# Kernel tuning notes

Hardware: AMD Instinct MI355X
Metric: run time of the kernel (lower is better)

Reference implementation:

```python
import jax, jax.numpy as jnp
import numpy as np

WINDOW = 128  # causal window width
D_SCALE = None  # set from val dim at trace time


def _softsign(x):
    return x / (1.0 + jnp.abs(x))


def setup_inputs() -> dict:
    key = jax.random.key(0)
    k1, k2 = jax.random.split(key)
    B, N, D = 4, 4096, 256
    val = jax.random.normal(k1, (B, N, D), dtype=jnp.float32)
    state = jax.random.normal(k2, (B, N), dtype=jnp.float32)
    return {"val": val, "state": state}


def reference(val, state):
    # val: [B, N, D], state: [B, N]
    B, N, D = val.shape
    # pairwise_fn: scaled dot product -> scores [B, N, N]
    scores = jnp.einsum('bnd,bmd->bnm', val, val) / jnp.sqrt(jnp.asarray(D, val.dtype))
    # edge_compress_fn: softsign
    edges = _softsign(scores)
    # causal window mask: source j satisfies (j <= i) & (j >= i - window)
    i = jnp.arange(N)[:, None]
    j = jnp.arange(N)[None, :]
    mask = (j <= i) & (j >= i - WINDOW)  # [N, N]
    edges = edges * mask[None, :, :].astype(edges.dtype)
    # val_proj_fn / state_proj_fn are Identity
    delta_state = jnp.einsum('bij,bj->bi', edges, state)   # [B, N]
    delta_val = jnp.einsum('bij,bjd->bid', edges, val)      # [B, N, D]
    return (delta_state, delta_val)
```

## Files before the change

### kernel.cpp

```cpp
#include <hip/hip_runtime.h>

#define NSEQ 4096
#define DIM  256
#define WIN  128
#define BATCH 4

typedef __bf16 bf16x8 __attribute__((ext_vector_type(8)));
typedef float  f32x4  __attribute__((ext_vector_type(4)));
typedef int    v2i    __attribute__((ext_vector_type(2)));
typedef int    v4i    __attribute__((ext_vector_type(4)));

__device__ __forceinline__ int sub_off(int j, int d) {
    return (((j >> 2) * 16 + (d >> 4)) << 6) + ((j & 3) << 4) + (d & 15);
}

__device__ __forceinline__ unsigned short f2bf(float f) {
    unsigned u = __builtin_bit_cast(unsigned, f);
    u += 0x7fffu + ((u >> 16) & 1u);
    return (unsigned short)(u >> 16);
}

__device__ __forceinline__ unsigned pk2bf(float lo, float hi) {
    unsigned r;
    asm("v_cvt_pk_bf16_f32 %0, %1, %2" : "=v"(r) : "v"(lo), "v"(hi));
    return r;
}

__global__ __launch_bounds__(256, 3)
void sp_kernel(const float* __restrict__ val,
               const float* __restrict__ state,
               float* __restrict__ out) {
    __shared__ __align__(128) unsigned short vbuf[2][8192];
    __shared__ __align__(128) unsigned short E_s[32 * 56];
    __shared__ float ds_part[4][16];

    const int bx  = blockIdx.x;
    const int lbx = ((bx & 7) << 6) + (bx >> 3);
    const int b      = lbx >> 7;
    const int tile_i = lbx & 127;
    const int r0     = tile_i << 5;

    const int t   = threadIdx.x;
    const int w   = t >> 6;
    const int l   = t & 63;
    const int l15 = l & 15;
    const int l4  = l >> 4;
    const int mt  = w >> 1;
    const int jt  = w & 1;

    const float* valb = val + ((size_t)b * NSEQ) * DIM;
    const float* stb  = state + ((size_t)b * NSEQ);
    float* out_state  = out + ((size_t)b * NSEQ);
    float* out_val    = out + (size_t)BATCH * NSEQ + ((size_t)b * NSEQ) * DIM;

    const int s_jl0 = (w << 2) + l4;
    const int s_jl1 = s_jl0 + 16;

    {
        const float* src = valb + ((size_t)tile_i << 13);
        #pragma unroll
        for (int qq = 0; qq < 8; ++qq) {
            const int jl = (qq & 1) ? s_jl1 : s_jl0;
            const int d0 = (l15 << 2) + ((qq >> 1) << 6);
            float4 v = *reinterpret_cast<const float4*>(src + jl * DIM + d0);
            uint2 u;
            u.x = pk2bf(v.x, v.y);
            u.y = pk2bf(v.z, v.w);
            *reinterpret_cast<uint2*>(&vbuf[0][sub_off(jl, d0)]) = u;
        }
    }
    __syncthreads();

    const int il = (mt << 4) + l15;
    const int jl = (jt << 4) + l15;
    bf16x8 af[8];
    #pragma unroll
    for (int ks = 0; ks < 8; ++ks)
        af[ks] = *reinterpret_cast<const bf16x8*>(&vbuf[0][sub_off(il, (l4 << 3) + (ks << 5))]);

    const int tj0   = (tile_i >= 4) ? (tile_i - 4) : 0;
    const int ntile = tile_i - tj0 + 1;

    float dsacc[4] = {0.f, 0.f, 0.f, 0.f};
    f32x4 accpv[2][4];
    #pragma unroll
    for (int m2 = 0; m2 < 2; ++m2)
        #pragma unroll
        for (int tt = 0; tt < 4; ++tt)
            accpv[m2][tt] = (f32x4){0.f, 0.f, 0.f, 0.f};

    int p = 0;
    for (int q = 0; q < ntile; ++q) {
        const int ti = tile_i - q;
        const bool havenext = (q + 1 < ntile);
        const unsigned short* bp = &vbuf[p][0];
        unsigned short* bn = &vbuf[1 - p][0];

        const int jg = (ti << 5) + jl;
        const float stv = stb[jg];

        bf16x8 sb[8];
        #pragma unroll
        for (int ks = 0; ks < 8; ++ks)
            sb[ks] = *reinterpret_cast<const bf16x8*>(&bp[sub_off(jl, (l4 << 3) + (ks << 5))]);
        f32x4 acc = (f32x4){0.f, 0.f, 0.f, 0.f};
        __builtin_amdgcn_s_setprio(1);
        #pragma unroll
        for (int ks = 0; ks < 8; ++ks)
            acc = __builtin_amdgcn_mfma_f32_16x16x32_bf16(af[ks], sb[ks], acc, 0, 0, 0);
        __builtin_amdgcn_s_setprio(0);

        const int ib = r0 + (mt << 4) + (l4 << 2);
        #pragma unroll
        for (int r = 0; r < 4; ++r) {
            float s = acc[r] * 0.0625f;
            float e = s * __builtin_amdgcn_rcpf(1.0f + fabsf(s));
            const int ig = ib + r;
            if (jg > ig || jg < ig - WIN) e = 0.0f;
            dsacc[r] += e * stv;
            E_s[((mt << 4) + (l4 << 2) + r) * 56 + (jt << 4) + l15] = f2bf(e);
        }

        if (havenext) {
            const float* src = valb + ((size_t)(ti - 1) << 13);
            #pragma unroll
            for (int qq = 0; qq < 8; ++qq) {
                const int jl2 = (qq & 1) ? s_jl1 : s_jl0;
                const int d0  = (l15 << 2) + ((qq >> 1) << 6);
                float4 v = *reinterpret_cast<const float4*>(src + jl2 * DIM + d0);
                uint2 u;
                u.x = pk2bf(v.x, v.y);
                u.y = pk2bf(v.z, v.w);
                *reinterpret_cast<uint2*>(&bn[sub_off(jl2, d0)]) = u;
            }
        }
        __syncthreads();

        bf16x8 ef0 = *reinterpret_cast<const bf16x8*>(&E_s[l15 * 56 + (l4 << 3)]);
        bf16x8 ef1 = *reinterpret_cast<const bf16x8*>(&E_s[(16 + l15) * 56 + (l4 << 3)]);
        const unsigned lds_base = (unsigned)(size_t)bp;
        v2i tr[8];
        #pragma unroll
        for (int tt = 0; tt < 4; ++tt) {
            const int nt = (w << 2) + tt;
            unsigned a0 = lds_base + (unsigned)((((l4 << 5) + nt) << 7) + (l15 << 3));
            asm volatile("ds_read_b64_tr_b16 %0, %1" : "=v"(tr[2 * tt]) : "v"(a0) : "memory");
            asm volatile("ds_read_b64_tr_b16 %0, %1 offset:2048" : "=v"(tr[2 * tt + 1]) : "v"(a0) : "memory");
        }
        asm volatile("s_waitcnt lgkmcnt(0)" ::: "memory");
        __builtin_amdgcn_sched_barrier(0);
        __builtin_amdgcn_s_setprio(1);
        #pragma unroll
        for (int tt = 0; tt < 4; ++tt) {
            v4i tmp;
            tmp.x = tr[2 * tt].x;     tmp.y = tr[2 * tt].y;
            tmp.z = tr[2 * tt + 1].x; tmp.w = tr[2 * tt + 1].y;
            bf16x8 bfr = __builtin_bit_cast(bf16x8, tmp);
            accpv[0][tt] = __builtin_amdgcn_mfma_f32_16x16x32_bf16(ef0, bfr, accpv[0][tt], 0, 0, 0);
            accpv[1][tt] = __builtin_amdgcn_mfma_f32_16x16x32_bf16(ef1, bfr, accpv[1][tt], 0, 0, 0);
        }
        __builtin_amdgcn_s_setprio(0);
        if (havenext) __syncthreads();
        p ^= 1;
    }

    #pragma unroll
    for (int m = 1; m <= 8; m <<= 1) {
        #pragma unroll
        for (int r = 0; r < 4; ++r)
            dsacc[r] += __shfl_xor(dsacc[r], m, 64);
    }
    if (l15 == 0) {
        #pragma unroll
        for (int r = 0; r < 4; ++r)
            ds_part[w][(l4 << 2) + r] = dsacc[r];
    }
    __syncthreads();
    if (t < 32) {
        const int m2 = t >> 4;
        out_state[r0 + t] = ds_part[(m2 << 1)][t & 15] + ds_part[(m2 << 1) + 1][t & 15];
    }

    #pragma unroll
    for (int m2 = 0; m2 < 2; ++m2) {
        #pragma unroll
        for (int tt = 0; tt < 4; ++tt) {
            const int d = (w << 6) + (tt << 4) + l15;
            #pragma unroll
            for (int r = 0; r < 4; ++r) {
                const int ig = r0 + (m2 << 4) + (l4 << 2) + r;
                out_val[(size_t)ig * DIM + d] = accpv[m2][tt][r];
            }
        }
    }
}

extern "C" void kernel_launch(void* const* d_in, const int* in_sizes, int n_in,
                              void* d_out, int out_size, void* d_ws, size_t ws_size,
                              hipStream_t stream) {
    const float* val   = (const float*)d_in[0];
    const float* state = (const float*)d_in[1];
    float* out = (float*)d_out;
    sp_kernel<<<dim3(BATCH * (NSEQ / 32)), dim3(256), 0, stream>>>(val, state, out);
}
```

Baseline: 16.53 us.

## Keep score tile in registers, drop E_s LDS round trip and mid-loop barrier

```diff
diff --git a/kernel.cpp b/kernel.cpp
--- a/kernel.cpp
+++ b/kernel.cpp
@@ -14,12 +14,6 @@
     return (((j >> 2) * 16 + (d >> 4)) << 6) + ((j & 3) << 4) + (d & 15);
 }
 
-__device__ __forceinline__ unsigned short f2bf(float f) {
-    unsigned u = __builtin_bit_cast(unsigned, f);
-    u += 0x7fffu + ((u >> 16) & 1u);
-    return (unsigned short)(u >> 16);
-}
-
 __device__ __forceinline__ unsigned pk2bf(float lo, float hi) {
     unsigned r;
     asm("v_cvt_pk_bf16_f32 %0, %1, %2" : "=v"(r) : "v"(lo), "v"(hi));
@@ -31,8 +25,6 @@
                const float* __restrict__ state,
                float* __restrict__ out) {
     __shared__ __align__(128) unsigned short vbuf[2][8192];
-    __shared__ __align__(128) unsigned short E_s[32 * 56];
-    __shared__ float ds_part[4][16];
 
     const int bx  = blockIdx.x;
     const int lbx = ((bx & 7) << 6) + (bx >> 3);
@@ -72,7 +64,6 @@
     __syncthreads();
 
     const int il = (mt << 4) + l15;
-    const int jl = (jt << 4) + l15;
     bf16x8 af[8];
     #pragma unroll
     for (int ks = 0; ks < 8; ++ks)
@@ -80,14 +71,13 @@
 
     const int tj0   = (tile_i >= 4) ? (tile_i - 4) : 0;
     const int ntile = tile_i - tj0 + 1;
+    const int ig    = r0 + (mt << 4) + l15;
 
-    float dsacc[4] = {0.f, 0.f, 0.f, 0.f};
-    f32x4 accpv[2][4];
+    float dsacc = 0.f;
+    f32x4 accpv[8];
     #pragma unroll
-    for (int m2 = 0; m2 < 2; ++m2)
-        #pragma unroll
-        for (int tt = 0; tt < 4; ++tt)
-            accpv[m2][tt] = (f32x4){0.f, 0.f, 0.f, 0.f};
+    for (int u = 0; u < 8; ++u)
+        accpv[u] = (f32x4){0.f, 0.f, 0.f, 0.f};
 
     int p = 0;
     for (int q = 0; q < ntile; ++q) {
@@ -95,31 +85,6 @@
         const bool havenext = (q + 1 < ntile);
         const unsigned short* bp = &vbuf[p][0];
         unsigned short* bn = &vbuf[1 - p][0];
-
-        const int jg = (ti << 5) + jl;
-        const float stv = stb[jg];
-
-        bf16x8 sb[8];
-        #pragma unroll
-        for (int ks = 0; ks < 8; ++ks)
-            sb[ks] = *reinterpret_cast<const bf16x8*>(&bp[sub_off(jl, (l4 << 3) + (ks << 5))]);
-        f32x4 acc = (f32x4){0.f, 0.f, 0.f, 0.f};
-        __builtin_amdgcn_s_setprio(1);
-        #pragma unroll
-        for (int ks = 0; ks < 8; ++ks)
-            acc = __builtin_amdgcn_mfma_f32_16x16x32_bf16(af[ks], sb[ks], acc, 0, 0, 0);
-        __builtin_amdgcn_s_setprio(0);
-
-        const int ib = r0 + (mt << 4) + (l4 << 2);
-        #pragma unroll
-        for (int r = 0; r < 4; ++r) {
-            float s = acc[r] * 0.0625f;
-            float e = s * __builtin_amdgcn_rcpf(1.0f + fabsf(s));
-            const int ig = ib + r;
-            if (jg > ig || jg < ig - WIN) e = 0.0f;
-            dsacc[r] += e * stv;
-            E_s[((mt << 4) + (l4 << 2) + r) * 56 + (jt << 4) + l15] = f2bf(e);
-        }
 
         if (havenext) {
             const float* src = valb + ((size_t)(ti - 1) << 13);
@@ -134,62 +99,89 @@
                 *reinterpret_cast<uint2*>(&bn[sub_off(jl2, d0)]) = u;
             }
         }
+
+        bf16x8 sb0[8], sb1[8];
+        #pragma unroll
+        for (int ks = 0; ks < 8; ++ks) {
+            sb0[ks] = *reinterpret_cast<const bf16x8*>(&bp[sub_off(l15,      (l4 << 3) + (ks << 5))]);
+            sb1[ks] = *reinterpret_cast<const bf16x8*>(&bp[sub_off(16 + l15, (l4 << 3) + (ks << 5))]);
+        }
+        f32x4 a0 = (f32x4){0.f, 0.f, 0.f, 0.f};
+        f32x4 a1 = (f32x4){0.f, 0.f, 0.f, 0.f};
+        #pragma unroll
+        for (int ks = 0; ks < 8; ++ks) {
+            a0 = __builtin_amdgcn_mfma_f32_16x16x32_bf16(sb0[ks], af[ks], a0, 0, 0, 0);
+            a1 = __builtin_amdgcn_mfma_f32_16x16x32_bf16(sb1[ks], af[ks], a1, 0, 0, 0);
+        }
+
+        const int jb = ti << 5;
+        const float4 st0 = *reinterpret_cast<const float4*>(stb + jb + (l4 << 2));
+        const float4 st1 = *reinterpret_cast<const float4*>(stb + jb + 16 + (l4 << 2));
+        float e0[4], e1[4];
+        #pragma unroll
+        for (int r = 0; r < 4; ++r) {
+            const int jg0 = jb + (l4 << 2) + r;
+            float s = a0[r] * 0.0625f;
+            float e = s * __builtin_amdgcn_rcpf(1.0f + fabsf(s));
+            if (jg0 > ig || jg0 < ig - WIN) e = 0.0f;
+            e0[r] = e;
+            const int jg1 = jg0 + 16;
+            s = a1[r] * 0.0625f;
+            e = s * __builtin_amdgcn_rcpf(1.0f + fabsf(s));
+            if (jg1 > ig || jg1 < ig - WIN) e = 0.0f;
+            e1[r] = e;
+        }
+        dsacc += e0[0] * st0.x + e0[1] * st0.y + e0[2] * st0.z + e0[3] * st0.w
+               + e1[0] * st1.x + e1[1] * st1.y + e1[2] * st1.z + e1[3] * st1.w;
+        v4i pw;
+        pw.x = pk2bf(e0[0], e0[1]);
+        pw.y = pk2bf(e0[2], e0[3]);
+        pw.z = pk2bf(e1[0], e1[1]);
+        pw.w = pk2bf(e1[2], e1[3]);
+        const bf16x8 pa = __builtin_bit_cast(bf16x8, pw);
+
+        const unsigned lds_base = (unsigned)(size_t)bp;
+        #pragma unroll
+        for (int g = 0; g < 2; ++g) {
+            v2i tr[8];
+            #pragma unroll
+            for (int tt = 0; tt < 4; ++tt) {
+                const int nt = (jt << 3) + (g << 2) + tt;
+                unsigned a0a = lds_base + (unsigned)((l4 << 11) + (nt << 7) + (l15 << 3));
+                asm volatile("ds_read_b64_tr_b16 %0, %1" : "=v"(tr[2 * tt]) : "v"(a0a) : "memory");
+                asm volatile("ds_read_b64_tr_b16 %0, %1 offset:8192" : "=v"(tr[2 * tt + 1]) : "v"(a0a) : "memory");
+            }
+            asm volatile("s_waitcnt lgkmcnt(0)" ::: "memory");
+            __builtin_amdgcn_sched_barrier(0);
+            #pragma unroll
+            for (int tt = 0; tt < 4; ++tt) {
+                v4i tmp;
+                tmp.x = tr[2 * tt].x;     tmp.y = tr[2 * tt].y;
+                tmp.z = tr[2 * tt + 1].x; tmp.w = tr[2 * tt + 1].y;
+                bf16x8 bfr = __builtin_bit_cast(bf16x8, tmp);
+                accpv[(g << 2) + tt] =
+                    __builtin_amdgcn_mfma_f32_16x16x32_bf16(pa, bfr, accpv[(g << 2) + tt], 0, 0, 0);
+            }
+        }
         __syncthreads();
-
-        bf16x8 ef0 = *reinterpret_cast<const bf16x8*>(&E_s[l15 * 56 + (l4 << 3)]);
-        bf16x8 ef1 = *reinterpret_cast<const bf16x8*>(&E_s[(16 + l15) * 56 + (l4 << 3)]);
-        const unsigned lds_base = (unsigned)(size_t)bp;
-        v2i tr[8];
-        #pragma unroll
-        for (int tt = 0; tt < 4; ++tt) {
-            const int nt = (w << 2) + tt;
-            unsigned a0 = lds_base + (unsigned)((((l4 << 5) + nt) << 7) + (l15 << 3));
-            asm volatile("ds_read_b64_tr_b16 %0, %1" : "=v"(tr[2 * tt]) : "v"(a0) : "memory");
-            asm volatile("ds_read_b64_tr_b16 %0, %1 offset:2048" : "=v"(tr[2 * tt + 1]) : "v"(a0) : "memory");
-        }
-        asm volatile("s_waitcnt lgkmcnt(0)" ::: "memory");
-        __builtin_amdgcn_sched_barrier(0);
-        __builtin_amdgcn_s_setprio(1);
-        #pragma unroll
-        for (int tt = 0; tt < 4; ++tt) {
-            v4i tmp;
-            tmp.x = tr[2 * tt].x;     tmp.y = tr[2 * tt].y;
-            tmp.z = tr[2 * tt + 1].x; tmp.w = tr[2 * tt + 1].y;
-            bf16x8 bfr = __builtin_bit_cast(bf16x8, tmp);
-            accpv[0][tt] = __builtin_amdgcn_mfma_f32_16x16x32_bf16(ef0, bfr, accpv[0][tt], 0, 0, 0);
-            accpv[1][tt] = __builtin_amdgcn_mfma_f32_16x16x32_bf16(ef1, bfr, accpv[1][tt], 0, 0, 0);
-        }
-        __builtin_amdgcn_s_setprio(0);
-        if (havenext) __syncthreads();
         p ^= 1;
     }
 
-    #pragma unroll
-    for (int m = 1; m <= 8; m <<= 1) {
-        #pragma unroll
-        for (int r = 0; r < 4; ++r)
-            dsacc[r] += __shfl_xor(dsacc[r], m, 64);
-    }
-    if (l15 == 0) {
-        #pragma unroll
-        for (int r = 0; r < 4; ++r)
-            ds_part[w][(l4 << 2) + r] = dsacc[r];
-    }
-    __syncthreads();
-    if (t < 32) {
-        const int m2 = t >> 4;
-        out_state[r0 + t] = ds_part[(m2 << 1)][t & 15] + ds_part[(m2 << 1) + 1][t & 15];
-    }
+    dsacc += __shfl_xor(dsacc, 16, 64);
+    dsacc += __shfl_xor(dsacc, 32, 64);
+    if (jt == 0 && l < 16)
+        out_state[r0 + (mt << 4) + l15] = dsacc;
 
     #pragma unroll
-    for (int m2 = 0; m2 < 2; ++m2) {
+    for (int g = 0; g < 2; ++g) {
         #pragma unroll
         for (int tt = 0; tt < 4; ++tt) {
-            const int d = (w << 6) + (tt << 4) + l15;
+            const int nt = (jt << 3) + (g << 2) + tt;
+            const int d  = (nt << 4) + l15;
             #pragma unroll
             for (int r = 0; r < 4; ++r) {
-                const int ig = r0 + (m2 << 4) + (l4 << 2) + r;
-                out_val[(size_t)ig * DIM + d] = accpv[m2][tt][r];
+                const int ig2 = r0 + (mt << 4) + (l4 << 2) + r;
+                out_val[(size_t)ig2 * DIM + d] = accpv[(g << 2) + tt][r];
             }
         }
     }
```

Result: slower. 19.16 us (+15.9%).

## Double row tile to 64 with 512 threads and preload all key tiles upfront

Applied to the files above, without the earlier changes.

```diff
diff --git a/kernel.cpp b/kernel.cpp
--- a/kernel.cpp
+++ b/kernel.cpp
@@ -26,19 +26,19 @@
     return r;
 }
 
-__global__ __launch_bounds__(256, 3)
+__global__ __launch_bounds__(512, 2)
 void sp_kernel(const float* __restrict__ val,
                const float* __restrict__ state,
                float* __restrict__ out) {
-    __shared__ __align__(128) unsigned short vbuf[2][8192];
-    __shared__ __align__(128) unsigned short E_s[32 * 56];
-    __shared__ float ds_part[4][16];
+    __shared__ __align__(128) unsigned short W[6 * 8192];
+    __shared__ __align__(128) unsigned short E_s[2][64 * 56];
+    __shared__ float ds_part[8][16];
 
     const int bx  = blockIdx.x;
-    const int lbx = ((bx & 7) << 6) + (bx >> 3);
-    const int b      = lbx >> 7;
-    const int tile_i = lbx & 127;
-    const int r0     = tile_i << 5;
+    const int lbx = ((bx & 7) << 5) + (bx >> 3);
+    const int b   = lbx >> 6;
+    const int i0  = (lbx & 63) << 6;
+    const int Ti  = (lbx & 63) << 1;
 
     const int t   = threadIdx.x;
     const int w   = t >> 6;
@@ -53,56 +53,58 @@
     float* out_state  = out + ((size_t)b * NSEQ);
     float* out_val    = out + (size_t)BATCH * NSEQ + ((size_t)b * NSEQ) * DIM;
 
-    const int s_jl0 = (w << 2) + l4;
-    const int s_jl1 = s_jl0 + 16;
+    const int Tj0   = (Ti >= 4) ? (Ti - 4) : 0;
+    const int ntile = Ti + 2 - Tj0;
 
     {
-        const float* src = valb + ((size_t)tile_i << 13);
-        #pragma unroll
-        for (int qq = 0; qq < 8; ++qq) {
-            const int jl = (qq & 1) ? s_jl1 : s_jl0;
-            const int d0 = (l15 << 2) + ((qq >> 1) << 6);
-            float4 v = *reinterpret_cast<const float4*>(src + jl * DIM + d0);
-            uint2 u;
-            u.x = pk2bf(v.x, v.y);
-            u.y = pk2bf(v.z, v.w);
-            *reinterpret_cast<uint2*>(&vbuf[0][sub_off(jl, d0)]) = u;
+        const int hh = t >> 8;
+        const int w4 = (t >> 6) & 3;
+        const int s_jl0 = (w4 << 2) + l4;
+        const int s_jl1 = s_jl0 + 16;
+        for (int k = 0; k < 3; ++k) {
+            const int s = hh + (k << 1);
+            if (s < ntile) {
+                const float* src = valb + ((size_t)(Tj0 + s) << 13);
+                unsigned short* dst = &W[s << 13];
+                #pragma unroll
+                for (int qq = 0; qq < 8; ++qq) {
+                    const int jl = (qq & 1) ? s_jl1 : s_jl0;
+                    const int d0 = (l15 << 2) + ((qq >> 1) << 6);
+                    float4 v = *reinterpret_cast<const float4*>(src + jl * DIM + d0);
+                    uint2 u;
+                    u.x = pk2bf(v.x, v.y);
+                    u.y = pk2bf(v.z, v.w);
+                    *reinterpret_cast<uint2*>(&dst[sub_off(jl, d0)]) = u;
+                }
+            }
         }
     }
     __syncthreads();
 
-    const int il = (mt << 4) + l15;
-    const int jl = (jt << 4) + l15;
+    const int slotVi = ntile - 2 + (mt >> 1);
+    const int ilr    = ((mt & 1) << 4) + l15;
     bf16x8 af[8];
     #pragma unroll
     for (int ks = 0; ks < 8; ++ks)
-        af[ks] = *reinterpret_cast<const bf16x8*>(&vbuf[0][sub_off(il, (l4 << 3) + (ks << 5))]);
-
-    const int tj0   = (tile_i >= 4) ? (tile_i - 4) : 0;
-    const int ntile = tile_i - tj0 + 1;
+        af[ks] = *reinterpret_cast<const bf16x8*>(&W[(slotVi << 13) + sub_off(ilr, (l4 << 3) + (ks << 5))]);
 
     float dsacc[4] = {0.f, 0.f, 0.f, 0.f};
-    f32x4 accpv[2][4];
+    f32x4 accpv[4][2];
     #pragma unroll
-    for (int m2 = 0; m2 < 2; ++m2)
+    for (int q = 0; q < 4; ++q)
         #pragma unroll
-        for (int tt = 0; tt < 4; ++tt)
-            accpv[m2][tt] = (f32x4){0.f, 0.f, 0.f, 0.f};
+        for (int u = 0; u < 2; ++u)
+            accpv[q][u] = (f32x4){0.f, 0.f, 0.f, 0.f};
 
-    int p = 0;
-    for (int q = 0; q < ntile; ++q) {
-        const int ti = tile_i - q;
-        const bool havenext = (q + 1 < ntile);
-        const unsigned short* bp = &vbuf[p][0];
-        unsigned short* bn = &vbuf[1 - p][0];
-
-        const int jg = (ti << 5) + jl;
-        const float stv = stb[jg];
+    for (int s = 0; s < ntile; ++s) {
+        const int jb = (Tj0 + s) << 5;
+        const unsigned short* bp = &W[s << 13];
+        unsigned short* Ec = &E_s[s & 1][0];
 
         bf16x8 sb[8];
         #pragma unroll
         for (int ks = 0; ks < 8; ++ks)
-            sb[ks] = *reinterpret_cast<const bf16x8*>(&bp[sub_off(jl, (l4 << 3) + (ks << 5))]);
+            sb[ks] = *reinterpret_cast<const bf16x8*>(&bp[sub_off((jt << 4) + l15, (l4 << 3) + (ks << 5))]);
         f32x4 acc = (f32x4){0.f, 0.f, 0.f, 0.f};
         __builtin_amdgcn_s_setprio(1);
         #pragma unroll
@@ -110,58 +112,47 @@
             acc = __builtin_amdgcn_mfma_f32_16x16x32_bf16(af[ks], sb[ks], acc, 0, 0, 0);
         __builtin_amdgcn_s_setprio(0);
 
-        const int ib = r0 + (mt << 4) + (l4 << 2);
+        const int jg = jb + (jt << 4) + l15;
+        const float stv = stb[jg];
         #pragma unroll
         for (int r = 0; r < 4; ++r) {
-            float s = acc[r] * 0.0625f;
-            float e = s * __builtin_amdgcn_rcpf(1.0f + fabsf(s));
-            const int ig = ib + r;
+            const int irow = (mt << 4) + (l4 << 2) + r;
+            const int ig   = i0 + irow;
+            float sv = acc[r] * 0.0625f;
+            float e  = sv * __builtin_amdgcn_rcpf(1.0f + fabsf(sv));
             if (jg > ig || jg < ig - WIN) e = 0.0f;
             dsacc[r] += e * stv;
-            E_s[((mt << 4) + (l4 << 2) + r) * 56 + (jt << 4) + l15] = f2bf(e);
-        }
-
-        if (havenext) {
-            const float* src = valb + ((size_t)(ti - 1) << 13);
-            #pragma unroll
-            for (int qq = 0; qq < 8; ++qq) {
-                const int jl2 = (qq & 1) ? s_jl1 : s_jl0;
-                const int d0  = (l15 << 2) + ((qq >> 1) << 6);
-                float4 v = *reinterpret_cast<const float4*>(src + jl2 * DIM + d0);
-                uint2 u;
-                u.x = pk2bf(v.x, v.y);
-                u.y = pk2bf(v.z, v.w);
-                *reinterpret_cast<uint2*>(&bn[sub_off(jl2, d0)]) = u;
-            }
+            Ec[irow * 56 + (jt << 4) + l15] = f2bf(e);
         }
         __syncthreads();
 
-        bf16x8 ef0 = *reinterpret_cast<const bf16x8*>(&E_s[l15 * 56 + (l4 << 3)]);
-        bf16x8 ef1 = *reinterpret_cast<const bf16x8*>(&E_s[(16 + l15) * 56 + (l4 << 3)]);
+        bf16x8 ef[4];
+        #pragma unroll
+        for (int q = 0; q < 4; ++q)
+            ef[q] = *reinterpret_cast<const bf16x8*>(&Ec[((q << 4) + l15) * 56 + (l4 << 3)]);
         const unsigned lds_base = (unsigned)(size_t)bp;
-        v2i tr[8];
+        v2i tr[4];
         #pragma unroll
-        for (int tt = 0; tt < 4; ++tt) {
-            const int nt = (w << 2) + tt;
+        for (int u = 0; u < 2; ++u) {
+            const int nt = (w << 1) + u;
             unsigned a0 = lds_base + (unsigned)((((l4 << 5) + nt) << 7) + (l15 << 3));
-            asm volatile("ds_read_b64_tr_b16 %0, %1" : "=v"(tr[2 * tt]) : "v"(a0) : "memory");
-            asm volatile("ds_read_b64_tr_b16 %0, %1 offset:2048" : "=v"(tr[2 * tt + 1]) : "v"(a0) : "memory");
+            asm volatile("ds_read_b64_tr_b16 %0, %1" : "=v"(tr[2 * u]) : "v"(a0) : "memory");
+            asm volatile("ds_read_b64_tr_b16 %0, %1 offset:2048" : "=v"(tr[2 * u + 1]) : "v"(a0) : "memory");
         }
         asm volatile("s_waitcnt lgkmcnt(0)" ::: "memory");
         __builtin_amdgcn_sched_barrier(0);
         __builtin_amdgcn_s_setprio(1);
         #pragma unroll
-        for (int tt = 0; tt < 4; ++tt) {
+        for (int u = 0; u < 2; ++u) {
             v4i tmp;
-            tmp.x = tr[2 * tt].x;     tmp.y = tr[2 * tt].y;
-            tmp.z = tr[2 * tt + 1].x; tmp.w = tr[2 * tt + 1].y;
+            tmp.x = tr[2 * u].x;     tmp.y = tr[2 * u].y;
+            tmp.z = tr[2 * u + 1].x; tmp.w = tr[2 * u + 1].y;
             bf16x8 bfr = __builtin_bit_cast(bf16x8, tmp);
-            accpv[0][tt] = __builtin_amdgcn_mfma_f32_16x16x32_bf16(ef0, bfr, accpv[0][tt], 0, 0, 0);
-            accpv[1][tt] = __builtin_amdgcn_mfma_f32_16x16x32_bf16(ef1, bfr, accpv[1][tt], 0, 0, 0);
+            #pragma unroll
+            for (int q = 0; q < 4; ++q)
+                accpv[q][u] = __builtin_amdgcn_mfma_f32_16x16x32_bf16(ef[q], bfr, accpv[q][u], 0, 0, 0);
         }
         __builtin_amdgcn_s_setprio(0);
-        if (havenext) __syncthreads();
-        p ^= 1;
     }
 
     #pragma unroll
@@ -176,20 +167,18 @@
             ds_part[w][(l4 << 2) + r] = dsacc[r];
     }
     __syncthreads();
-    if (t < 32) {
-        const int m2 = t >> 4;
-        out_state[r0 + t] = ds_part[(m2 << 1)][t & 15] + ds_part[(m2 << 1) + 1][t & 15];
-    }
+    if (t < 64)
+        out_state[i0 + t] = ds_part[(t >> 4) << 1][t & 15] + ds_part[((t >> 4) << 1) + 1][t & 15];
 
     #pragma unroll
-    for (int m2 = 0; m2 < 2; ++m2) {
+    for (int q = 0; q < 4; ++q) {
         #pragma unroll
-        for (int tt = 0; tt < 4; ++tt) {
-            const int d = (w << 6) + (tt << 4) + l15;
+        for (int u = 0; u < 2; ++u) {
+            const int d = (((w << 1) + u) << 4) + l15;
             #pragma unroll
             for (int r = 0; r < 4; ++r) {
-                const int ig = r0 + (m2 << 4) + (l4 << 2) + r;
-                out_val[(size_t)ig * DIM + d] = accpv[m2][tt][r];
+                const int ig = i0 + (q << 4) + (l4 << 2) + r;
+                out_val[(size_t)ig * DIM + d] = accpv[q][u][r];
             }
         }
     }
@@ -201,5 +190,5 @@
     const float* val   = (const float*)d_in[0];
     const float* state = (const float*)d_in[1];
     float* out = (float*)d_out;
-    sp_kernel<<<dim3(BATCH * (NSEQ / 32)), dim3(256), 0, stream>>>(val, state, out);
+    sp_kernel<<<dim3(BATCH * (NSEQ / 64)), dim3(512), 0, stream>>>(val, state, out);
 }
```

After: 16.79 us. No clear change (+1.6%).

## Pre-convert val to swizzled bf16 workspace and stream tiles via global_load_lds

Applied to the files above, without the earlier changes.

```diff
diff --git a/kernel.cpp b/kernel.cpp
--- a/kernel.cpp
+++ b/kernel.cpp
@@ -26,8 +26,41 @@
     return r;
 }
 
+__device__ __forceinline__ void gload16(const void* g, void* l) {
+    __builtin_amdgcn_global_load_lds(
+        (const __attribute__((address_space(1))) unsigned int*)g,
+        (__attribute__((address_space(3))) unsigned int*)l, 16, 0, 0);
+}
+
+__global__ __launch_bounds__(256)
+void cvt_kernel(const float* __restrict__ val, unsigned short* __restrict__ wsA) {
+    __shared__ unsigned short A_l[8192];
+    const int tile = blockIdx.x;
+    const float* src = val + ((size_t)tile << 13);
+    const int t = threadIdx.x;
+    const int j = t >> 3;
+    const int dbase = (t & 7) << 2;
+
+    #pragma unroll
+    for (int p = 0; p < 8; ++p) {
+        const int d = dbase + (p << 5);
+        float4 v = *reinterpret_cast<const float4*>(src + j * 256 + d);
+        uint2 u;
+        u.x = pk2bf(v.x, v.y);
+        u.y = pk2bf(v.z, v.w);
+        *reinterpret_cast<uint2*>(&A_l[sub_off(j, d)]) = u;
+    }
+    __syncthreads();
+    unsigned short* dstA = wsA + ((size_t)tile << 13);
+    #pragma unroll
+    for (int i = 0; i < 4; ++i) {
+        uint4 x = *reinterpret_cast<const uint4*>(&A_l[(i << 11) + (t << 3)]);
+        *reinterpret_cast<uint4*>(dstA + (i << 11) + (t << 3)) = x;
+    }
+}
+
 __global__ __launch_bounds__(256, 3)
-void sp_kernel(const float* __restrict__ val,
+void sp_kernel(const unsigned short* __restrict__ wsA,
                const float* __restrict__ state,
                float* __restrict__ out) {
     __shared__ __align__(128) unsigned short vbuf[2][8192];
@@ -48,25 +81,16 @@
     const int mt  = w >> 1;
     const int jt  = w & 1;
 
-    const float* valb = val + ((size_t)b * NSEQ) * DIM;
     const float* stb  = state + ((size_t)b * NSEQ);
     float* out_state  = out + ((size_t)b * NSEQ);
     float* out_val    = out + (size_t)BATCH * NSEQ + ((size_t)b * NSEQ) * DIM;
 
-    const int s_jl0 = (w << 2) + l4;
-    const int s_jl1 = s_jl0 + 16;
-
     {
-        const float* src = valb + ((size_t)tile_i << 13);
-        #pragma unroll
-        for (int qq = 0; qq < 8; ++qq) {
-            const int jl = (qq & 1) ? s_jl1 : s_jl0;
-            const int d0 = (l15 << 2) + ((qq >> 1) << 6);
-            float4 v = *reinterpret_cast<const float4*>(src + jl * DIM + d0);
-            uint2 u;
-            u.x = pk2bf(v.x, v.y);
-            u.y = pk2bf(v.z, v.w);
-            *reinterpret_cast<uint2*>(&vbuf[0][sub_off(jl, d0)]) = u;
+        const char* g = (const char*)wsA + (((size_t)((b << 7) + tile_i)) << 14);
+        #pragma unroll
+        for (int k = 0; k < 4; ++k) {
+            const int off = ((w << 2) + k) << 10;
+            gload16(g + off + (l << 4), ((char*)&vbuf[0][0]) + off);
         }
     }
     __syncthreads();
@@ -95,6 +119,15 @@
         const bool havenext = (q + 1 < ntile);
         const unsigned short* bp = &vbuf[p][0];
         unsigned short* bn = &vbuf[1 - p][0];
+
+        if (havenext) {
+            const char* g = (const char*)wsA + (((size_t)((b << 7) + ti - 1)) << 14);
+            #pragma unroll
+            for (int k = 0; k < 4; ++k) {
+                const int off = ((w << 2) + k) << 10;
+                gload16(g + off + (l << 4), ((char*)bn) + off);
+            }
+        }
 
         const int jg = (ti << 5) + jl;
         const float stv = stb[jg];
@@ -120,20 +153,6 @@
             dsacc[r] += e * stv;
             E_s[((mt << 4) + (l4 << 2) + r) * 56 + (jt << 4) + l15] = f2bf(e);
         }
-
-        if (havenext) {
-            const float* src = valb + ((size_t)(ti - 1) << 13);
-            #pragma unroll
-            for (int qq = 0; qq < 8; ++qq) {
-                const int jl2 = (qq & 1) ? s_jl1 : s_jl0;
-                const int d0  = (l15 << 2) + ((qq >> 1) << 6);
-                float4 v = *reinterpret_cast<const float4*>(src + jl2 * DIM + d0);
-                uint2 u;
-                u.x = pk2bf(v.x, v.y);
-                u.y = pk2bf(v.z, v.w);
-                *reinterpret_cast<uint2*>(&bn[sub_off(jl2, d0)]) = u;
-            }
-        }
         __syncthreads();
 
         bf16x8 ef0 = *reinterpret_cast<const bf16x8*>(&E_s[l15 * 56 + (l4 << 3)]);
@@ -201,5 +220,8 @@
     const float* val   = (const float*)d_in[0];
     const float* state = (const float*)d_in[1];
     float* out = (float*)d_out;
-    sp_kernel<<<dim3(BATCH * (NSEQ / 32)), dim3(256), 0, stream>>>(val, state, out);
-}
+    unsigned short* wsA = (unsigned short*)d_ws;
+
+    cvt_kernel<<<dim3(BATCH * 128), dim3(256), 0, stream>>>(val, wsA);
+    sp_kernel<<<dim3(BATCH * 128), dim3(256), 0, stream>>>(wsA, state, out);
+}
```

After: 23.03 us. 39.3% more time.
